# Kernel tuning notes

Hardware: AMD Instinct MI355X
Metric: run time of the kernel (lower is better)

The kernel has to match this reference:

```python
import jax, jax.numpy as jnp
import numpy as np

B, S, D = 4, 2048, 1024
H = 16
DH = D // H


def setup_inputs() -> dict:
    key = jax.random.key(0)
    ks = jax.random.split(key, 5)
    scale = 1.0 / np.sqrt(D)
    return {
        "x": jax.random.normal(ks[0], (B, S, D), dtype=jnp.float32),
        "wq": jax.random.normal(ks[1], (D, D), dtype=jnp.float32) * scale,
        "wk": jax.random.normal(ks[2], (D, D), dtype=jnp.float32) * scale,
        "wv": jax.random.normal(ks[3], (D, D), dtype=jnp.float32) * scale,
        "wo": jax.random.normal(ks[4], (D, D), dtype=jnp.float32) * scale,
    }


def reference(x, wq, wk, wv, wo):
    b, s, d = x.shape
    # nn.Linear applies x @ W.T (weights are [out, in])
    q = (x @ wq.T).reshape(b, s, H, DH).transpose(0, 2, 1, 3)  # [b,h,s,dh]
    k = (x @ wk.T).reshape(b, s, H, DH).transpose(0, 2, 1, 3)
    v = (x @ wv.T).reshape(b, s, H, DH).transpose(0, 2, 1, 3)
    scale = 1.0 / jnp.sqrt(jnp.asarray(DH, dtype=x.dtype))
    scores = jnp.einsum("bhqd,bhkd->bhqk", q, k) * scale  # [b,h,s,s]
    causal = jnp.tril(jnp.ones((s, s), dtype=bool))
    scores = jnp.where(causal, scores, -jnp.inf)
    attn = jax.nn.softmax(scores, axis=-1)
    out = jnp.einsum("bhqk,bhkd->bhqd", attn, v)  # [b,h,s,dh]
    out = out.transpose(0, 2, 1, 3).reshape(b, s, d)
    return out @ wo.T
```

## Files before the change

kernel.cpp:

```cpp
#include <hip/hip_runtime.h>
#include <hip/hip_bf16.h>

#define Bz 4
#define Sz 2048
#define Dz 1024
#define Hz 16
#define DHz 64

typedef __bf16 bf16x8 __attribute__((ext_vector_type(8)));
typedef float f32x4 __attribute__((ext_vector_type(4)));
typedef short s16x4 __attribute__((ext_vector_type(4)));
typedef unsigned short u16x4 __attribute__((ext_vector_type(4)));

#define SCQF 0.18033688011112042f

__global__ __launch_bounds__(256) void cvt_all(const float* __restrict__ x,
                                               const float* __restrict__ w0, const float* __restrict__ w1,
                                               const float* __restrict__ w2, const float* __restrict__ w3,
                                               __hip_bfloat16* __restrict__ dst) {
    constexpr int TOK = Bz * Sz * Dz;
    constexpr int WEL = Dz * Dz;
    int i = (blockIdx.x * 256 + threadIdx.x) * 4;
    const float* src;
    if (i < TOK) {
        src = x + i;
    } else {
        const int jj = i - TOK;
        const int which = jj >> 20;
        const float* w = (which == 0) ? w0 : (which == 1) ? w1 : (which == 2) ? w2 : w3;
        src = w + (jj & (WEL - 1));
    }
    float4 f = *reinterpret_cast<const float4*>(src);
    dst[i + 0] = __float2bfloat16(f.x);
    dst[i + 1] = __float2bfloat16(f.y);
    dst[i + 2] = __float2bfloat16(f.z);
    dst[i + 3] = __float2bfloat16(f.w);
}

__device__ __forceinline__ void gl2lds16(const __hip_bfloat16* g, __hip_bfloat16* l) {
    __builtin_amdgcn_global_load_lds(
        (const __attribute__((address_space(1))) void*)g,
        (__attribute__((address_space(3))) void*)l, 16, 0, 0);
}

__device__ __forceinline__ unsigned ldsaddr(const void* p) {
    return (unsigned)(size_t)(const __attribute__((address_space(3))) void*)p;
}

template <int N, int K, typename OT, int MODE, bool SCQ = false>
__device__ __forceinline__ void gemm128_body(const __hip_bfloat16* __restrict__ A,
                                             const __hip_bfloat16* __restrict__ W,
                                             OT* __restrict__ C, int bm, int bn,
                                             __hip_bfloat16* As, __hip_bfloat16* Bs) {
    const int tid  = threadIdx.x;
    const int wid  = tid >> 6;
    const int lane = tid & 63;
    const int quad = lane >> 4;
    const int l16  = lane & 15;
    const int wr = wid >> 1, wc = wid & 1;

    const int rlo = lane >> 3;
    const int xel = ((lane & 7) ^ rlo) * 8;
    const __hip_bfloat16* gA = A + (size_t)(bm * 128 + wid * 32 + rlo) * K + xel;
    const __hip_bfloat16* gB = W + (size_t)(bn * 128 + wid * 32 + rlo) * K + xel;
    __hip_bfloat16* lA = &As[(wid * 32) * 64];
    __hip_bfloat16* lB = &Bs[(wid * 32) * 64];

    const unsigned sw = (unsigned)((l16 & 7) << 4);
    const char* Ap = (const char*)As;
    const char* Bp = (const char*)Bs;

    f32x4 acc[4][4] = {};

    for (int k0 = 0; k0 < K; k0 += 64) {
        __syncthreads();
#pragma unroll
        for (int c = 0; c < 4; ++c) {
            gl2lds16(gA + (size_t)(c * 8) * K + k0, lA + (c * 8) * 64);
            gl2lds16(gB + (size_t)(c * 8) * K + k0, lB + (c * 8) * 64);
        }
        __syncthreads();

#pragma unroll
        for (int kk = 0; kk < 2; ++kk) {
            bf16x8 af[4], bf[4];
#pragma unroll
            for (int mi = 0; mi < 4; ++mi)
                af[mi] = *reinterpret_cast<const bf16x8*>(
                    Ap + (wr * 64 + mi * 16 + l16) * 128 + ((kk * 64 + quad * 16) ^ sw));
#pragma unroll
            for (int ni = 0; ni < 4; ++ni)
                bf[ni] = *reinterpret_cast<const bf16x8*>(
                    Bp + (wc * 64 + ni * 16 + l16) * 128 + ((kk * 64 + quad * 16) ^ sw));
#pragma unroll
            for (int mi = 0; mi < 4; ++mi)
#pragma unroll
                for (int ni = 0; ni < 4; ++ni)
                    acc[mi][ni] = __builtin_amdgcn_mfma_f32_16x16x32_bf16(af[mi], bf[ni], acc[mi][ni], 0, 0, 0);
        }
    }

#pragma unroll
    for (int mi = 0; mi < 4; ++mi)
#pragma unroll
        for (int ni = 0; ni < 4; ++ni) {
            const int row0 = bm * 128 + wr * 64 + mi * 16 + quad * 4;
            const int col  = bn * 128 + wc * 64 + ni * 16 + l16;
#pragma unroll
            for (int r = 0; r < 4; ++r) {
                const int row = row0 + r;
                float v = acc[mi][ni][r];
                if constexpr (SCQ) v *= SCQF;
                if constexpr (MODE == 0) {
                    if constexpr (__is_same(OT, float))
                        C[(size_t)row * N + col] = v;
                    else
                        C[(size_t)row * N + col] = __float2bfloat16(v);
                } else if constexpr (MODE == 1) {
                    const int bh = (row >> 11) * Hz + (col >> 6);
                    C[(size_t)bh * (Sz * DHz) + (size_t)(row & 2047) * 64 + (col & 63)] =
                        __float2bfloat16(v);
                } else {
                    const int bh = (row >> 11) * Hz + (col >> 6);
                    C[(size_t)bh * (Sz * DHz) + (size_t)((col >> 4) & 3) * (Sz * 16) +
                      (size_t)(row & 2047) * 16 + (col & 15)] = __float2bfloat16(v);
                }
            }
        }
}

template <int M, int N, int K, typename OT>
__global__ __launch_bounds__(256) void gemm128(const __hip_bfloat16* __restrict__ A,
                                               const __hip_bfloat16* __restrict__ W,
                                               OT* __restrict__ C) {
    __shared__ __hip_bfloat16 As[128 * 64];
    __shared__ __hip_bfloat16 Bs[128 * 64];
    constexpr int NB = N / 128;
    gemm128_body<N, K, OT, 0>(A, W, C, blockIdx.x / NB, blockIdx.x % NB, As, Bs);
}

template <int M, int K>
__global__ __launch_bounds__(256) void gemm_qkv(const __hip_bfloat16* __restrict__ A,
                                                const __hip_bfloat16* __restrict__ W0,
                                                const __hip_bfloat16* __restrict__ W1,
                                                const __hip_bfloat16* __restrict__ W2,
                                                __hip_bfloat16* __restrict__ C0,
                                                __hip_bfloat16* __restrict__ C1,
                                                __hip_bfloat16* __restrict__ C2) {
    __shared__ __hip_bfloat16 As[128 * 64];
    __shared__ __hip_bfloat16 Bs[128 * 64];
    constexpr int NB = Dz / 128;
    const int which = blockIdx.x % 3;
    const int rem   = blockIdx.x / 3;
    const int bm = rem / NB, bn = rem % NB;
    if (which == 0)      gemm128_body<Dz, K, __hip_bfloat16, 0, true>(A, W0, C0, bm, bn, As, Bs);
    else if (which == 1) gemm128_body<Dz, K, __hip_bfloat16, 1>(A, W1, C1, bm, bn, As, Bs);
    else                 gemm128_body<Dz, K, __hip_bfloat16, 2>(A, W2, C2, bm, bn, As, Bs);
}

__device__ __forceinline__ f32x4 mfma16bf(s16x4 a, s16x4 b, f32x4 c) {
#if __has_builtin(__builtin_amdgcn_mfma_f32_16x16x16bf16_1k)
    return __builtin_amdgcn_mfma_f32_16x16x16bf16_1k(a, b, c, 0, 0, 0);
#else
    asm volatile("v_mfma_f32_16x16x16_bf16 %0, %1, %2, %0" : "+v"(c) : "v"(a), "v"(b));
    return c;
#endif
}

#define TRD(i, off) \
    asm volatile("ds_read_b64_tr_b16 %0, %1 offset:" off : "=v"(vf[i]) : "v"(va))

__global__ __launch_bounds__(256, 4) void attn_mfma7(const __hip_bfloat16* __restrict__ Q,
                                                     const __hip_bfloat16* __restrict__ Kh,
                                                     const __hip_bfloat16* __restrict__ Vh,
                                                     __hip_bfloat16* __restrict__ O) {
    __shared__ __hip_bfloat16 Ks[2][64 * 64];
    __shared__ __hip_bfloat16 Vs[2][64 * 64];

    const int tid  = threadIdx.x;
    const int wid  = tid >> 6;
    const int lane = tid & 63;
    const int quad = lane >> 4;
    const int l16  = lane & 15;

    const int xcd  = blockIdx.x & 7;
    const int j    = blockIdx.x >> 3;
    const int bh   = xcd * 8 + (j >> 4);
    const int pair = j & 15;
    const int h    = bh & 15;
    const int b    = bh >> 4;
    const size_t baseQ = (size_t)b * Sz * Dz + (size_t)h * DHz;
    const size_t kvb   = (size_t)bh * (Sz * DHz);

    const int rlo = lane >> 3;
    const int xel = ((lane & 7) ^ rlo) * 8;

    auto stage = [&](int kn, int bf_) {
#pragma unroll
        for (int c = 0; c < 2; ++c) {
            gl2lds16(Kh + kvb + (size_t)(kn + wid * 16 + c * 8 + rlo) * 64 + xel,
                     &Ks[bf_][(wid * 16 + c * 8) * 64]);
            gl2lds16(Vh + kvb + (size_t)wid * (Sz * 16) + (size_t)(kn + c * 32 + (lane >> 1)) * 16 + (lane & 1) * 8,
                     &Vs[bf_][wid * 1024 + c * 512]);
        }
    };

    const unsigned vb0 = ldsaddr(&Vs[0][0]) + lane * 8;
    const unsigned sw  = (l16 & 7) << 4;

    const s16x4 ones = {(short)0x3F80, (short)0x3F80, (short)0x3F80, (short)0x3F80};

    int buf = 0;
    stage(0, 0);
    __syncthreads();

#pragma unroll 1
    for (int p = 0; p < 2; ++p) {
        const int qblk  = (p == 0) ? pair : 31 - pair;
        const int q0    = qblk * 64 + wid * 16;
        const int niter = qblk + 1;

        const __hip_bfloat16* qp = Q + baseQ + (size_t)(q0 + l16) * Dz + quad * 8;
        const bf16x8 qf0 = *reinterpret_cast<const bf16x8*>(qp);
        const bf16x8 qf1 = *reinterpret_cast<const bf16x8*>(qp + 32);

        float m = -1e30f;
        f32x4 ot[4] = {};
        f32x4 lacc  = {};

#pragma unroll 1
        for (int it = 0; it < niter; ++it) {
            const int k0 = it * 64;

            f32x4 st[4] = {};
            {
                const char* Kp = (const char*)&Ks[buf][0];
#pragma unroll
                for (int s = 0; s < 4; ++s) {
                    const int rb = (s * 16 + l16) * 128;
                    const bf16x8 a0 = *reinterpret_cast<const bf16x8*>(Kp + rb + ((quad * 16) ^ sw));
                    const bf16x8 a1 = *reinterpret_cast<const bf16x8*>(Kp + rb + ((quad * 16 + 64) ^ sw));
                    st[s] = __builtin_amdgcn_mfma_f32_16x16x32_bf16(a0, qf0, st[s], 0, 0, 0);
                    st[s] = __builtin_amdgcn_mfma_f32_16x16x32_bf16(a1, qf1, st[s], 0, 0, 0);
                }
            }

            const bool more = (it + 1 < niter);
            if (more)        stage(k0 + 64, buf ^ 1);
            else if (p == 0) stage(0,       buf ^ 1);

            float sv[16];
            if (it == niter - 1) {
                const int qrow = q0 + l16;
#pragma unroll
                for (int s = 0; s < 4; ++s)
#pragma unroll
                    for (int r = 0; r < 4; ++r) {
                        const int key = k0 + s * 16 + quad * 4 + r;
                        sv[s * 4 + r] = (key <= qrow) ? st[s][r] : -1e30f;
                    }
            } else {
#pragma unroll
                for (int s = 0; s < 4; ++s)
#pragma unroll
                    for (int r = 0; r < 4; ++r) sv[s * 4 + r] = st[s][r];
            }

            const float p0 = fmaxf(fmaxf(sv[0],  sv[1]),  sv[2]);
            const float p1 = fmaxf(fmaxf(sv[3],  sv[4]),  sv[5]);
            const float p2 = fmaxf(fmaxf(sv[6],  sv[7]),  sv[8]);
            const float p3 = fmaxf(fmaxf(sv[9],  sv[10]), sv[11]);
            const float p4 = fmaxf(fmaxf(sv[12], sv[13]), sv[14]);
            const float p5 = fmaxf(fmaxf(p0, p1), p2);
            float tmax = fmaxf(fmaxf(fmaxf(p5, p3), p4), sv[15]);
            tmax = fmaxf(tmax, __shfl_xor(tmax, 16, 64));
            tmax = fmaxf(tmax, __shfl_xor(tmax, 32, 64));

            const float mnew = fmaxf(m, tmax);
            const bool  skip = __all(tmax <= m);
            if (!skip) {
                const float alpha = __builtin_amdgcn_exp2f(m - mnew);
                m = mnew;
#pragma unroll
                for (int s = 0; s < 4; ++s) ot[s] *= alpha;
                lacc[0] *= alpha;
            }

            float pv[16];
#pragma unroll
            for (int i = 0; i < 16; ++i) pv[i] = __builtin_amdgcn_exp2f(sv[i] - m);

            s16x4 vf[16];
            const unsigned va = vb0 + (unsigned)(buf << 13);
            TRD(0, "0");    TRD(1, "512");  TRD(2, "1024"); TRD(3, "1536");
            TRD(4, "2048"); TRD(5, "2560"); TRD(6, "3072"); TRD(7, "3584");

            s16x4 pw[4];
#pragma unroll
            for (int s = 0; s < 4; ++s)
#pragma unroll
                for (int r = 0; r < 4; ++r) {
                    union { __hip_bfloat16 hh; short uu; } cv;
                    cv.hh = __float2bfloat16(pv[s * 4 + r]);
                    pw[s][r] = cv.uu;
                }

            lacc = mfma16bf(ones, pw[0], lacc);
            lacc = mfma16bf(ones, pw[1], lacc);
            lacc = mfma16bf(ones, pw[2], lacc);
            lacc = mfma16bf(ones, pw[3], lacc);

            asm volatile("s_waitcnt lgkmcnt(0)" ::: "memory");
            __builtin_amdgcn_sched_barrier(0);
            TRD(8,  "4096"); TRD(9,  "4608"); TRD(10, "5120"); TRD(11, "5632");
            TRD(12, "6144"); TRD(13, "6656"); TRD(14, "7168"); TRD(15, "7680");

            ot[0] = mfma16bf(vf[0],  pw[0], ot[0]);
            ot[0] = mfma16bf(vf[1],  pw[1], ot[0]);
            ot[0] = mfma16bf(vf[2],  pw[2], ot[0]);
            ot[0] = mfma16bf(vf[3],  pw[3], ot[0]);
            ot[1] = mfma16bf(vf[4],  pw[0], ot[1]);
            ot[1] = mfma16bf(vf[5],  pw[1], ot[1]);
            ot[1] = mfma16bf(vf[6],  pw[2], ot[1]);
            ot[1] = mfma16bf(vf[7],  pw[3], ot[1]);

            asm volatile("s_waitcnt lgkmcnt(0)" ::: "memory");
            __builtin_amdgcn_sched_barrier(0);
            ot[2] = mfma16bf(vf[8],  pw[0], ot[2]);
            ot[2] = mfma16bf(vf[9],  pw[1], ot[2]);
            ot[2] = mfma16bf(vf[10], pw[2], ot[2]);
            ot[2] = mfma16bf(vf[11], pw[3], ot[2]);
            ot[3] = mfma16bf(vf[12], pw[0], ot[3]);
            ot[3] = mfma16bf(vf[13], pw[1], ot[3]);
            ot[3] = mfma16bf(vf[14], pw[2], ot[3]);
            ot[3] = mfma16bf(vf[15], pw[3], ot[3]);

            __syncthreads();
            buf ^= 1;
        }

        const float linv = 1.f / lacc[0];
        __hip_bfloat16* op = O + baseQ + (size_t)(q0 + l16) * Dz + quad * 4;
#pragma unroll
        for (int sd = 0; sd < 4; ++sd) {
            u16x4 w;
#pragma unroll
            for (int r = 0; r < 4; ++r) {
                union { __hip_bfloat16 hh; unsigned short uu; } cv;
                cv.hh = __float2bfloat16(ot[sd][r] * linv);
                w[r] = cv.uu;
            }
            *reinterpret_cast<u16x4*>(op + sd * 16) = w;
        }
    }
}

extern "C" void kernel_launch(void* const* d_in, const int* in_sizes, int n_in,
                              void* d_out, int out_size, void* d_ws, size_t ws_size,
                              hipStream_t stream) {
    const float* x  = (const float*)d_in[0];
    const float* wq = (const float*)d_in[1];
    const float* wk = (const float*)d_in[2];
    const float* wv = (const float*)d_in[3];
    const float* wo = (const float*)d_in[4];
    float* out = (float*)d_out;

    constexpr int TOK = Bz * Sz * Dz;
    constexpr int WEL = Dz * Dz;

    __hip_bfloat16* xb  = (__hip_bfloat16*)d_ws;
    __hip_bfloat16* wqb = xb  + TOK;
    __hip_bfloat16* wkb = wqb + WEL;
    __hip_bfloat16* wvb = wkb + WEL;
    __hip_bfloat16* wob = wvb + WEL;
    __hip_bfloat16* Qb  = wob + WEL;
    __hip_bfloat16* Kh  = Qb + TOK;
    __hip_bfloat16* Vh  = (__hip_bfloat16*)d_out;
    __hip_bfloat16* Ob  = xb;

    cvt_all<<<(TOK + 4 * WEL) / 4 / 256, 256, 0, stream>>>(x, wq, wk, wv, wo, xb);

    constexpr int M = Bz * Sz;
    constexpr int GB = (M / 128) * (Dz / 128);

    gemm_qkv<M, Dz><<<3 * GB, 256, 0, stream>>>(xb, wqb, wkb, wvb, Qb, Kh, Vh);

    const int ATTN_BLOCKS = Bz * Hz * 16;
    attn_mfma7<<<ATTN_BLOCKS, 256, 0, stream>>>(Qb, Kh, Vh, Ob);

    gemm128<M, Dz, Dz, float><<<GB, 256, 0, stream>>>(Ob, wob, out);
}
```

Baseline: 237.2 us.

## Split paired causal query blocks into separate heavy-first attention blocks

Each attention block previously handled a pair of query blocks (i and 31-i) to balance causal work; now each block handles a single query block, launched in descending-work order (heaviest first), doubling the grid. The launch bound is raised to 5 waves per SIMD, K fragments are loaded before the MFMAs, and the next tile's prefetch is issued before the QK compute. MFMA sections are wrapped in s_setprio to favour matrix issue across waves. Intent is better occupancy and scheduling-based load balance, at the cost of more blocks, reloading the first K/V tile per block, and possible register spills under the tighter launch bound.

Result: slower. 249.7 us (+5.3%).

```diff
diff --git a/kernel.cpp b/kernel.cpp
--- a/kernel.cpp
+++ b/kernel.cpp
@@ -170,7 +170,7 @@
 #define TRD(i, off) \
     asm volatile("ds_read_b64_tr_b16 %0, %1 offset:" off : "=v"(vf[i]) : "v"(va))
 
-__global__ __launch_bounds__(256, 4) void attn_mfma7(const __hip_bfloat16* __restrict__ Q,
+__global__ __launch_bounds__(256, 5) void attn_mfma8(const __hip_bfloat16* __restrict__ Q,
                                                      const __hip_bfloat16* __restrict__ Kh,
                                                      const __hip_bfloat16* __restrict__ Vh,
                                                      __hip_bfloat16* __restrict__ O) {
@@ -185,8 +185,8 @@
 
     const int xcd  = blockIdx.x & 7;
     const int j    = blockIdx.x >> 3;
-    const int bh   = xcd * 8 + (j >> 4);
-    const int pair = j & 15;
+    const int bh   = xcd * 8 + (j >> 5);
+    const int qblk = 31 - (j & 31);
     const int h    = bh & 15;
     const int b    = bh >> 4;
     const size_t baseQ = (size_t)b * Sz * Dz + (size_t)h * DHz;
@@ -210,148 +210,154 @@
 
     const s16x4 ones = {(short)0x3F80, (short)0x3F80, (short)0x3F80, (short)0x3F80};
 
+    const int q0    = qblk * 64 + wid * 16;
+    const int niter = qblk + 1;
+
+    const __hip_bfloat16* qp = Q + baseQ + (size_t)(q0 + l16) * Dz + quad * 8;
+    const bf16x8 qf0 = *reinterpret_cast<const bf16x8*>(qp);
+    const bf16x8 qf1 = *reinterpret_cast<const bf16x8*>(qp + 32);
+
+    float m = -1e30f;
+    f32x4 ot[4] = {};
+    f32x4 lacc  = {};
+
     int buf = 0;
     stage(0, 0);
     __syncthreads();
 
 #pragma unroll 1
-    for (int p = 0; p < 2; ++p) {
-        const int qblk  = (p == 0) ? pair : 31 - pair;
-        const int q0    = qblk * 64 + wid * 16;
-        const int niter = qblk + 1;
-
-        const __hip_bfloat16* qp = Q + baseQ + (size_t)(q0 + l16) * Dz + quad * 8;
-        const bf16x8 qf0 = *reinterpret_cast<const bf16x8*>(qp);
-        const bf16x8 qf1 = *reinterpret_cast<const bf16x8*>(qp + 32);
-
-        float m = -1e30f;
-        f32x4 ot[4] = {};
-        f32x4 lacc  = {};
-
-#pragma unroll 1
-        for (int it = 0; it < niter; ++it) {
-            const int k0 = it * 64;
-
-            f32x4 st[4] = {};
-            {
-                const char* Kp = (const char*)&Ks[buf][0];
-#pragma unroll
-                for (int s = 0; s < 4; ++s) {
-                    const int rb = (s * 16 + l16) * 128;
-                    const bf16x8 a0 = *reinterpret_cast<const bf16x8*>(Kp + rb + ((quad * 16) ^ sw));
-                    const bf16x8 a1 = *reinterpret_cast<const bf16x8*>(Kp + rb + ((quad * 16 + 64) ^ sw));
-                    st[s] = __builtin_amdgcn_mfma_f32_16x16x32_bf16(a0, qf0, st[s], 0, 0, 0);
-                    st[s] = __builtin_amdgcn_mfma_f32_16x16x32_bf16(a1, qf1, st[s], 0, 0, 0);
+    for (int it = 0; it < niter; ++it) {
+        const int k0 = it * 64;
+
+        if (it + 1 < niter) stage(k0 + 64, buf ^ 1);
+
+        f32x4 st[4] = {};
+        {
+            const char* Kp = (const char*)&Ks[buf][0];
+            bf16x8 a0[4], a1[4];
+#pragma unroll
+            for (int s = 0; s < 4; ++s) {
+                const int rb = (s * 16 + l16) * 128;
+                a0[s] = *reinterpret_cast<const bf16x8*>(Kp + rb + ((quad * 16) ^ sw));
+                a1[s] = *reinterpret_cast<const bf16x8*>(Kp + rb + ((quad * 16 + 64) ^ sw));
+            }
+            __builtin_amdgcn_s_setprio(1);
+#pragma unroll
+            for (int s = 0; s < 4; ++s) {
+                st[s] = __builtin_amdgcn_mfma_f32_16x16x32_bf16(a0[s], qf0, st[s], 0, 0, 0);
+                st[s] = __builtin_amdgcn_mfma_f32_16x16x32_bf16(a1[s], qf1, st[s], 0, 0, 0);
+            }
+            __builtin_amdgcn_s_setprio(0);
+        }
+
+        float sv[16];
+        if (it == niter - 1) {
+            const int qrow = q0 + l16;
+#pragma unroll
+            for (int s = 0; s < 4; ++s)
+#pragma unroll
+                for (int r = 0; r < 4; ++r) {
+                    const int key = k0 + s * 16 + quad * 4 + r;
+                    sv[s * 4 + r] = (key <= qrow) ? st[s][r] : -1e30f;
                 }
+        } else {
+#pragma unroll
+            for (int s = 0; s < 4; ++s)
+#pragma unroll
+                for (int r = 0; r < 4; ++r) sv[s * 4 + r] = st[s][r];
+        }
+
+        const float p0 = fmaxf(fmaxf(sv[0],  sv[1]),  sv[2]);
+        const float p1 = fmaxf(fmaxf(sv[3],  sv[4]),  sv[5]);
+        const float p2 = fmaxf(fmaxf(sv[6],  sv[7]),  sv[8]);
+        const float p3 = fmaxf(fmaxf(sv[9],  sv[10]), sv[11]);
+        const float p4 = fmaxf(fmaxf(sv[12], sv[13]), sv[14]);
+        const float p5 = fmaxf(fmaxf(p0, p1), p2);
+        float tmax = fmaxf(fmaxf(fmaxf(p5, p3), p4), sv[15]);
+        tmax = fmaxf(tmax, __shfl_xor(tmax, 16, 64));
+        tmax = fmaxf(tmax, __shfl_xor(tmax, 32, 64));
+
+        const float mnew = fmaxf(m, tmax);
+        const bool  skip = __all(tmax <= m);
+        if (!skip) {
+            const float alpha = __builtin_amdgcn_exp2f(m - mnew);
+            m = mnew;
+#pragma unroll
+            for (int s = 0; s < 4; ++s) ot[s] *= alpha;
+            lacc[0] *= alpha;
+        }
+
+        float pv[16];
+#pragma unroll
+        for (int i = 0; i < 16; ++i) pv[i] = __builtin_amdgcn_exp2f(sv[i] - m);
+
+        s16x4 vf[16];
+        const unsigned va = vb0 + (unsigned)(buf << 13);
+        TRD(0, "0");    TRD(1, "512");  TRD(2, "1024"); TRD(3, "1536");
+        TRD(4, "2048"); TRD(5, "2560"); TRD(6, "3072"); TRD(7, "3584");
+
+        s16x4 pw[4];
+#pragma unroll
+        for (int s = 0; s < 4; ++s)
+#pragma unroll
+            for (int r = 0; r < 4; ++r) {
+                union { __hip_bfloat16 hh; short uu; } cv;
+                cv.hh = __float2bfloat16(pv[s * 4 + r]);
+                pw[s][r] = cv.uu;
             }
 
-            const bool more = (it + 1 < niter);
-            if (more)        stage(k0 + 64, buf ^ 1);
-            else if (p == 0) stage(0,       buf ^ 1);
-
-            float sv[16];
-            if (it == niter - 1) {
-                const int qrow = q0 + l16;
-#pragma unroll
-                for (int s = 0; s < 4; ++s)
-#pragma unroll
-                    for (int r = 0; r < 4; ++r) {
-                        const int key = k0 + s * 16 + quad * 4 + r;
-                        sv[s * 4 + r] = (key <= qrow) ? st[s][r] : -1e30f;
-                    }
-            } else {
-#pragma unroll
-                for (int s = 0; s < 4; ++s)
-#pragma unroll
-                    for (int r = 0; r < 4; ++r) sv[s * 4 + r] = st[s][r];
-            }
-
-            const float p0 = fmaxf(fmaxf(sv[0],  sv[1]),  sv[2]);
-            const float p1 = fmaxf(fmaxf(sv[3],  sv[4]),  sv[5]);
-            const float p2 = fmaxf(fmaxf(sv[6],  sv[7]),  sv[8]);
-            const float p3 = fmaxf(fmaxf(sv[9],  sv[10]), sv[11]);
-            const float p4 = fmaxf(fmaxf(sv[12], sv[13]), sv[14]);
-            const float p5 = fmaxf(fmaxf(p0, p1), p2);
-            float tmax = fmaxf(fmaxf(fmaxf(p5, p3), p4), sv[15]);
-            tmax = fmaxf(tmax, __shfl_xor(tmax, 16, 64));
-            tmax = fmaxf(tmax, __shfl_xor(tmax, 32, 64));
-
-            const float mnew = fmaxf(m, tmax);
-            const bool  skip = __all(tmax <= m);
-            if (!skip) {
-                const float alpha = __builtin_amdgcn_exp2f(m - mnew);
-                m = mnew;
-#pragma unroll
-                for (int s = 0; s < 4; ++s) ot[s] *= alpha;
-                lacc[0] *= alpha;
-            }
-
-            float pv[16];
-#pragma unroll
-            for (int i = 0; i < 16; ++i) pv[i] = __builtin_amdgcn_exp2f(sv[i] - m);
-
-            s16x4 vf[16];
-            const unsigned va = vb0 + (unsigned)(buf << 13);
-            TRD(0, "0");    TRD(1, "512");  TRD(2, "1024"); TRD(3, "1536");
-            TRD(4, "2048"); TRD(5, "2560"); TRD(6, "3072"); TRD(7, "3584");
-
-            s16x4 pw[4];
-#pragma unroll
-            for (int s = 0; s < 4; ++s)
-#pragma unroll
-                for (int r = 0; r < 4; ++r) {
-                    union { __hip_bfloat16 hh; short uu; } cv;
-                    cv.hh = __float2bfloat16(pv[s * 4 + r]);
-                    pw[s][r] = cv.uu;
-                }
-
-            lacc = mfma16bf(ones, pw[0], lacc);
-            lacc = mfma16bf(ones, pw[1], lacc);
-            lacc = mfma16bf(ones, pw[2], lacc);
-            lacc = mfma16bf(ones, pw[3], lacc);
-
-            asm volatile("s_waitcnt lgkmcnt(0)" ::: "memory");
-            __builtin_amdgcn_sched_barrier(0);
-            TRD(8,  "4096"); TRD(9,  "4608"); TRD(10, "5120"); TRD(11, "5632");
-            TRD(12, "6144"); TRD(13, "6656"); TRD(14, "7168"); TRD(15, "7680");
-
-            ot[0] = mfma16bf(vf[0],  pw[0], ot[0]);
-            ot[0] = mfma16bf(vf[1],  pw[1], ot[0]);
-            ot[0] = mfma16bf(vf[2],  pw[2], ot[0]);
-            ot[0] = mfma16bf(vf[3],  pw[3], ot[0]);
-            ot[1] = mfma16bf(vf[4],  pw[0], ot[1]);
-            ot[1] = mfma16bf(vf[5],  pw[1], ot[1]);
-            ot[1] = mfma16bf(vf[6],  pw[2], ot[1]);
-            ot[1] = mfma16bf(vf[7],  pw[3], ot[1]);
-
-            asm volatile("s_waitcnt lgkmcnt(0)" ::: "memory");
-            __builtin_amdgcn_sched_barrier(0);
-            ot[2] = mfma16bf(vf[8],  pw[0], ot[2]);
-            ot[2] = mfma16bf(vf[9],  pw[1], ot[2]);
-            ot[2] = mfma16bf(vf[10], pw[2], ot[2]);
-            ot[2] = mfma16bf(vf[11], pw[3], ot[2]);
-            ot[3] = mfma16bf(vf[12], pw[0], ot[3]);
-            ot[3] = mfma16bf(vf[13], pw[1], ot[3]);
-            ot[3] = mfma16bf(vf[14], pw[2], ot[3]);
-            ot[3] = mfma16bf(vf[15], pw[3], ot[3]);
-
-            __syncthreads();
-            buf ^= 1;
-        }
-
-        const float linv = 1.f / lacc[0];
-        __hip_bfloat16* op = O + baseQ + (size_t)(q0 + l16) * Dz + quad * 4;
-#pragma unroll
-        for (int sd = 0; sd < 4; ++sd) {
-            u16x4 w;
-#pragma unroll
-            for (int r = 0; r < 4; ++r) {
-                union { __hip_bfloat16 hh; unsigned short uu; } cv;
-                cv.hh = __float2bfloat16(ot[sd][r] * linv);
-                w[r] = cv.uu;
-            }
-            *reinterpret_cast<u16x4*>(op + sd * 16) = w;
-        }
+        __builtin_amdgcn_s_setprio(1);
+        lacc = mfma16bf(ones, pw[0], lacc);
+        lacc = mfma16bf(ones, pw[1], lacc);
+        lacc = mfma16bf(ones, pw[2], lacc);
+        lacc = mfma16bf(ones, pw[3], lacc);
+        __builtin_amdgcn_s_setprio(0);
+
+        asm volatile("s_waitcnt lgkmcnt(0)" ::: "memory");
+        __builtin_amdgcn_sched_barrier(0);
+        TRD(8,  "4096"); TRD(9,  "4608"); TRD(10, "5120"); TRD(11, "5632");
+        TRD(12, "6144"); TRD(13, "6656"); TRD(14, "7168"); TRD(15, "7680");
+
+        __builtin_amdgcn_s_setprio(1);
+        ot[0] = mfma16bf(vf[0],  pw[0], ot[0]);
+        ot[0] = mfma16bf(vf[1],  pw[1], ot[0]);
+        ot[0] = mfma16bf(vf[2],  pw[2], ot[0]);
+        ot[0] = mfma16bf(vf[3],  pw[3], ot[0]);
+        ot[1] = mfma16bf(vf[4],  pw[0], ot[1]);
+        ot[1] = mfma16bf(vf[5],  pw[1], ot[1]);
+        ot[1] = mfma16bf(vf[6],  pw[2], ot[1]);
+        ot[1] = mfma16bf(vf[7],  pw[3], ot[1]);
+        __builtin_amdgcn_s_setprio(0);
+
+        asm volatile("s_waitcnt lgkmcnt(0)" ::: "memory");
+        __builtin_amdgcn_sched_barrier(0);
+        __builtin_amdgcn_s_setprio(1);
+        ot[2] = mfma16bf(vf[8],  pw[0], ot[2]);
+        ot[2] = mfma16bf(vf[9],  pw[1], ot[2]);
+        ot[2] = mfma16bf(vf[10], pw[2], ot[2]);
+        ot[2] = mfma16bf(vf[11], pw[3], ot[2]);
+        ot[3] = mfma16bf(vf[12], pw[0], ot[3]);
+        ot[3] = mfma16bf(vf[13], pw[1], ot[3]);
+        ot[3] = mfma16bf(vf[14], pw[2], ot[3]);
+        ot[3] = mfma16bf(vf[15], pw[3], ot[3]);
+        __builtin_amdgcn_s_setprio(0);
+
+        __syncthreads();
+        buf ^= 1;
+    }
+
+    const float linv = 1.f / lacc[0];
+    __hip_bfloat16* op = O + baseQ + (size_t)(q0 + l16) * Dz + quad * 4;
+#pragma unroll
+    for (int sd = 0; sd < 4; ++sd) {
+        u16x4 w;
+#pragma unroll
+        for (int r = 0; r < 4; ++r) {
+            union { __hip_bfloat16 hh; unsigned short uu; } cv;
+            cv.hh = __float2bfloat16(ot[sd][r] * linv);
+            w[r] = cv.uu;
+        }
+        *reinterpret_cast<u16x4*>(op + sd * 16) = w;
     }
 }
 
@@ -385,8 +391,8 @@
 
     gemm_qkv<M, Dz><<<3 * GB, 256, 0, stream>>>(xb, wqb, wkb, wvb, Qb, Kh, Vh);
 
-    const int ATTN_BLOCKS = Bz * Hz * 16;
-    attn_mfma7<<<ATTN_BLOCKS, 256, 0, stream>>>(Qb, Kh, Vh, Ob);
+    const int ATTN_BLOCKS = Bz * Hz * 32;
+    attn_mfma8<<<ATTN_BLOCKS, 256, 0, stream>>>(Qb, Kh, Vh, Ob);
 
     gemm128<M, Dz, Dz, float><<<GB, 256, 0, stream>>>(Ob, wob, out);
 }
```
